# Kernel optimization log

Hardware: AMD Instinct MI355X
Metric: run time of the kernel (lower is better)

The kernel has to match this reference:

```python
import jax, jax.numpy as jnp
import numpy as np

B, SEQ, S, DIM_IN, DIM_K, DIM_V = 4, 2048, 128, 512, 64, 64
L = SEQ + 2 * S
NEG = -1e30  # stand-in for log(0) in the tril mask (finite for stable vjp)


def _layernorm(x, g, b, eps=1e-5):
    m = jnp.mean(x, axis=-1, keepdims=True)
    v = jnp.var(x, axis=-1, keepdims=True)
    return (x - m) / jnp.sqrt(v + eps) * g + b


def setup_inputs() -> dict:
    key = jax.random.key(0)
    ks = jax.random.split(key, 18)
    w = lambda k, shape, s=0.02: (jax.random.normal(k, shape, jnp.float32) * s)
    inp = {
        "x": jax.random.normal(ks[0], (B, L, DIM_IN), jnp.float32),
        "Wq": w(ks[1], (DIM_IN, DIM_K)),
        "Wk": w(ks[2], (DIM_IN, DIM_K)),
        "Wv": w(ks[3], (DIM_IN, DIM_V)),
        "Wq_s": w(ks[4], (DIM_IN, DIM_K)),
        "Wk_s": w(ks[5], (DIM_IN, DIM_K)),
        "Wv_s": w(ks[6], (DIM_IN, DIM_V)),
        "Wq_e": w(ks[7], (DIM_IN, DIM_K)),
        "Wk_e": w(ks[8], (DIM_IN, DIM_K)),
        "Wv_e": w(ks[9], (DIM_IN, DIM_V)),
        "ln_g": jnp.ones((DIM_IN,), jnp.float32),
        "ln_b": jnp.zeros((DIM_IN,), jnp.float32),
        "ln_s_g": jnp.ones((DIM_IN,), jnp.float32),
        "ln_s_b": jnp.zeros((DIM_IN,), jnp.float32),
        "ln_e_g": jnp.ones((DIM_IN,), jnp.float32),
        "ln_e_b": jnp.zeros((DIM_IN,), jnp.float32),
        "cope_emb": jax.random.normal(ks[10], (DIM_K, S), jnp.float32),
        "offset": 0,
    }
    return inp


def reference(x, Wq, Wk, Wv, Wq_s, Wk_s, Wv_s, Wq_e, Wk_e, Wv_e,
              ln_g, ln_b, ln_s_g, ln_s_b, ln_e_g, ln_e_b, cope_emb, offset):
    # extract_state: first/last state_len tokens
    xs, xm, xe = x[:, :S], x[:, S:L - S], x[:, -S:]
    xm = _layernorm(xm, ln_g, ln_b)
    xs = _layernorm(xs, ln_s_g, ln_s_b)
    xe = _layernorm(xe, ln_e_g, ln_e_b)

    q, k, v = xm @ Wq, xm @ Wk, xm @ Wv          # (B, SEQ, dk/dv)
    q_s, k_s, v_s = xs @ Wq_s, xs @ Wk_s, xs @ Wv_s
    q_e, k_e, v_e = xe @ Wq_e, xe @ Wk_e, xe @ Wv_e

    # CoPE bias over the non-state block
    logits = jnp.einsum('bqd,bkd->bqk', q, k)    # (B, SEQ, SEQ)
    gates = jax.nn.sigmoid(logits)
    pos = jnp.flip(jnp.cumsum(jnp.flip(gates, -1), axis=-1), -1)
    pos = jnp.minimum(pos, jnp.float32(S - 1))
    pos_ceil = jnp.ceil(pos).astype(jnp.int32)
    pos_floor = jnp.floor(pos).astype(jnp.int32)
    logits_int = jnp.einsum('bqd,dk->bqk', q, cope_emb)  # (B, SEQ, S)
    logits_c = jnp.take_along_axis(logits_int, pos_ceil, axis=-1)
    logits_f = jnp.take_along_axis(logits_int, pos_floor, axis=-1)
    wfrac = pos - pos_floor.astype(pos.dtype)
    bias = logits_c * wfrac + logits_f * (1.0 - wfrac)   # (B, SEQ, SEQ)

    q_full = jnp.concatenate([q_s, q, q_e], axis=1)      # (B, L, dk)
    k_full = jnp.concatenate([k_s, k, k_e], axis=1)
    v_full = jnp.concatenate([v_s, v, v_e], axis=1)

    # explicit tril log-mask bias with CoPE injected in the middle block
    tri = jnp.tril(jnp.ones((L, L), dtype=bool))
    attn_bias = jnp.where(tri, 0.0, NEG).astype(jnp.float32)
    attn_bias = jnp.broadcast_to(attn_bias, (B, L, L))
    attn_bias = attn_bias.at[:, S:L - S, S:L - S].add(bias)

    scale = 1.0 / jnp.sqrt(jnp.float32(DIM_K))
    scores = jnp.einsum('bqd,bkd->bqk', q_full, k_full) * scale + attn_bias
    att = jax.nn.softmax(scores, axis=-1)
    return jnp.einsum('bqk,bkd->bqd', att, v_full)       # (B, L, dv)
```

## Files before the change

kernel.cpp:

```cpp
#include <hip/hip_runtime.h>
#include <math.h>

#define B_    4
#define SEQ_  2048
#define S_    128
#define L_    2304
#define DIN   512
#define DK    64
#define NEGINF (-1e30f)
#define SCALE 0.125f
#define NCOLS 2176
#define NMID  8192
#define NEDGE 1024
#define LE    2304

typedef _Float16 f16;
typedef __attribute__((ext_vector_type(8))) _Float16 half8;
typedef __attribute__((ext_vector_type(4))) float f32x4;

union U4 { uint4 u; f16 h[8]; };

__global__ __launch_bounds__(256) void k_wsplit(
    const float* __restrict__ Wq,  const float* __restrict__ Wk,  const float* __restrict__ Wv,
    const float* __restrict__ Wqs, const float* __restrict__ Wks, const float* __restrict__ Wvs,
    const float* __restrict__ Wqe, const float* __restrict__ Wke, const float* __restrict__ Wve,
    f16* __restrict__ Wsp)
{
    __shared__ float xs[64 * 68];
    const int kt  = blockIdx.x;
    const int mat = blockIdx.y;
    const float* W;
    switch (mat) {
        case 0: W = Wq;  break; case 1: W = Wk;  break; case 2: W = Wv;  break;
        case 3: W = Wqs; break; case 4: W = Wks; break; case 5: W = Wvs; break;
        case 6: W = Wqe; break; case 7: W = Wke; break; default: W = Wve; break;
    }
    const int tid = threadIdx.x;
    const int k0  = kt * 64;
    #pragma unroll
    for (int i = 0; i < 4; ++i) {
        int g = tid + 256 * i;
        int k = g >> 4, c4 = g & 15;
        *(float4*)(xs + k * 68 + c4 * 4) = ((const float4*)W)[(size_t)(k0 + k) * 16 + c4];
    }
    __syncthreads();
    const int col = tid & 63, hf = tid >> 6;
    const int kk0 = hf * 16;
    U4 hi0, hi1, lo0, lo1;
    #pragma unroll
    for (int j = 0; j < 8; ++j) {
        float v0 = xs[(kk0 + j) * 68 + col];
        float v1 = xs[(kk0 + 8 + j) * 68 + col];
        hi0.h[j] = (f16)v0; lo0.h[j] = (f16)(v0 - (float)hi0.h[j]);
        hi1.h[j] = (f16)v1; lo1.h[j] = (f16)(v1 - (float)hi1.h[j]);
    }
    f16* dst = Wsp + (size_t)mat * 65536 + (size_t)col * 1024 + k0 + kk0;
    *(uint4*)(dst)       = hi0.u;
    *(uint4*)(dst + 8)   = hi1.u;
    *(uint4*)(dst + 512) = lo0.u;
    *(uint4*)(dst + 520) = lo1.u;
}

__global__ __launch_bounds__(256) void k_proj(
    const float* __restrict__ x, const f16* __restrict__ Wsp,
    const float* __restrict__ g0, const float* __restrict__ b0,
    const float* __restrict__ gs, const float* __restrict__ bs,
    const float* __restrict__ ge, const float* __restrict__ be,
    f16* __restrict__ qsp, f16* __restrict__ ksp, f16* __restrict__ vhT)
{
    __shared__ f16 As[32 * 136];
    __shared__ f16 Bs[3 * 64 * 136];
    __shared__ float mean_s[32], rstd_s[32];
    const int tid  = threadIdx.x;
    const int row0 = blockIdx.x * 32;
    const int rseq = row0 % L_;
    const int seg  = (rseq < S_) ? 0 : (rseq >= L_ - S_) ? 2 : 1;
    const int mat0 = (seg == 0) ? 3 : (seg == 2) ? 6 : 0;
    const float* gg = (seg == 0) ? gs : (seg == 2) ? ge : g0;
    const float* bb = (seg == 0) ? bs : (seg == 2) ? be : b0;

    {
        const int rr = tid >> 3, qq = tid & 7;
        const float4* xr = (const float4*)(x + (size_t)(row0 + rr) * DIN) + qq * 16;
        float s = 0.f, s2 = 0.f;
        #pragma unroll
        for (int i = 0; i < 16; ++i) {
            float4 v = xr[i];
            s  += v.x + v.y + v.z + v.w;
            s2 += v.x * v.x + v.y * v.y + v.z * v.z + v.w * v.w;
        }
        s  += __shfl_xor(s, 1);  s  += __shfl_xor(s, 2);  s  += __shfl_xor(s, 4);
        s2 += __shfl_xor(s2, 1); s2 += __shfl_xor(s2, 2); s2 += __shfl_xor(s2, 4);
        if (qq == 0) {
            float mean = s * (1.f / DIN);
            mean_s[rr] = mean;
            rstd_s[rr] = rsqrtf(s2 * (1.f / DIN) - mean * mean + 1e-5f);
        }
    }

    const int w = tid >> 6, lane = tid & 63;
    const int cl = lane & 15, quad = lane >> 4;
    const int r0 = 16 * (w >> 1), c0 = 32 * (w & 1);

    f32x4 acc[3][2];
    #pragma unroll
    for (int m = 0; m < 3; ++m)
        #pragma unroll
        for (int j = 0; j < 2; ++j) acc[m][j] = 0.f;

    for (int kc = 0; kc < DIN; kc += 64) {
        __syncthreads();
        {
            int r = tid >> 3, c8 = tid & 7;
            const float* xp = x + (size_t)(row0 + r) * DIN + kc + c8 * 8;
            float4 a0 = *(const float4*)xp;
            float4 a1 = *(const float4*)(xp + 4);
            float4 gA = *(const float4*)(gg + kc + c8 * 8);
            float4 gB = *(const float4*)(gg + kc + c8 * 8 + 4);
            float4 bA = *(const float4*)(bb + kc + c8 * 8);
            float4 bB = *(const float4*)(bb + kc + c8 * 8 + 4);
            float mean = mean_s[r], rstd = rstd_s[r];
            float n[8];
            n[0] = (a0.x - mean) * rstd * gA.x + bA.x;
            n[1] = (a0.y - mean) * rstd * gA.y + bA.y;
            n[2] = (a0.z - mean) * rstd * gA.z + bA.z;
            n[3] = (a0.w - mean) * rstd * gA.w + bA.w;
            n[4] = (a1.x - mean) * rstd * gB.x + bB.x;
            n[5] = (a1.y - mean) * rstd * gB.y + bB.y;
            n[6] = (a1.z - mean) * rstd * gB.z + bB.z;
            n[7] = (a1.w - mean) * rstd * gB.w + bB.w;
            U4 hi, lo;
            #pragma unroll
            for (int j = 0; j < 8; ++j) {
                hi.h[j] = (f16)n[j];
                lo.h[j] = (f16)(n[j] - (float)hi.h[j]);
            }
            *(uint4*)(As + r * 136 + c8 * 8)      = hi.u;
            *(uint4*)(As + r * 136 + 64 + c8 * 8) = lo.u;
        }
        #pragma unroll
        for (int i = 0; i < 6; ++i) {
            int g = tid + 256 * i;
            int mm = g >> 9, rem = g & 511;
            int col = rem >> 3, c8 = rem & 7;
            const f16* src = Wsp + (size_t)(mat0 + mm) * 65536 + (size_t)col * 1024 + kc + c8 * 8;
            f16* dst = Bs + mm * 8704 + col * 136 + c8 * 8;
            *(uint4*)(dst)      = *(const uint4*)(src);
            *(uint4*)(dst + 64) = *(const uint4*)(src + 512);
        }
        __syncthreads();
        #pragma unroll
        for (int h = 0; h < 2; ++h) {
            half8 ah, al;
            {
                const f16* base = As + (r0 + cl) * 136 + h * 32 + quad * 8;
                ah = *(const half8*)(base);
                al = *(const half8*)(base + 64);
            }
            #pragma unroll
            for (int m = 0; m < 3; ++m)
                #pragma unroll
                for (int cs = 0; cs < 2; ++cs) {
                    const f16* base = Bs + m * 8704 + (c0 + 16 * cs + cl) * 136 + h * 32 + quad * 8;
                    half8 bh = *(const half8*)(base);
                    half8 bl = *(const half8*)(base + 64);
                    acc[m][cs] = __builtin_amdgcn_mfma_f32_16x16x32_f16(ah, bh, acc[m][cs], 0, 0, 0);
                    acc[m][cs] = __builtin_amdgcn_mfma_f32_16x16x32_f16(ah, bl, acc[m][cs], 0, 0, 0);
                    acc[m][cs] = __builtin_amdgcn_mfma_f32_16x16x32_f16(al, bh, acc[m][cs], 0, 0, 0);
                }
        }
    }

    const int bI = row0 / L_;
    const int rb = row0 - bI * L_;
    #pragma unroll
    for (int m = 0; m < 3; ++m) {
        f16* sp = (m == 0) ? qsp : ksp;
        #pragma unroll
        for (int cs = 0; cs < 2; ++cs)
            #pragma unroll
            for (int r = 0; r < 4; ++r) {
                int lrow = r0 + quad * 4 + r;
                int col  = c0 + 16 * cs + cl;
                float v  = acc[m][cs][r];
                size_t grow = (size_t)(row0 + lrow);
                if (m < 2) {
                    f16 hv = (f16)v;
                    sp[grow * 128 + col]      = hv;
                    sp[grow * 128 + 64 + col] = (f16)(v - (float)hv);
                } else {
                    vhT[(size_t)(bI * 64 + col) * L_ + rb + lrow] = (f16)v;
                }
            }
    }
}

__global__ __launch_bounds__(256) void k_dots(
    const f16* __restrict__ qsp, const f16* __restrict__ ksp,
    float* __restrict__ D32, float* __restrict__ G, float* __restrict__ De32)
{
    const int bx = blockIdx.x, by = blockIdx.y;
    const bool edge = (bx >= 64);
    int b, q0 = 0;
    size_t qrow0;
    if (!edge) {
        if (by >= 17) return;
        b = bx >> 4;
        q0 = (bx * 128) & 2047;
        qrow0 = (size_t)b * L_ + S_ + q0;
    } else {
        int ex = bx - 64;
        b = ex >> 1;
        int half = ex & 1;
        if (half == 0 && by > 0) return;
        qrow0 = (size_t)b * L_ + (half ? 2176 : 0);
    }
    const int col0 = by * 128;
    const size_t krow0 = (size_t)b * L_ + col0;

    __shared__ f16 Qs[128 * 136];
    __shared__ f16 Ks[128 * 136];
    const int tid = threadIdx.x;

    #pragma unroll
    for (int i = 0; i < 8; ++i) {
        int g = tid + 256 * i;
        int r = g >> 4, c = g & 15;
        *(uint4*)(Qs + r * 136 + c * 8) = *(const uint4*)(qsp + (qrow0 + r) * 128 + c * 8);
        *(uint4*)(Ks + r * 136 + c * 8) = *(const uint4*)(ksp + (krow0 + r) * 128 + c * 8);
    }
    __syncthreads();

    const int w = tid >> 6, lane = tid & 63;
    const int cl = lane & 15, quad = lane >> 4;

    f32x4 acc[2][8];
    #pragma unroll
    for (int i = 0; i < 2; ++i)
        #pragma unroll
        for (int j = 0; j < 8; ++j) acc[i][j] = 0.f;

    #pragma unroll
    for (int h = 0; h < 2; ++h) {
        half8 ah[2], al[2];
        #pragma unroll
        for (int rs = 0; rs < 2; ++rs) {
            const f16* base = Qs + (32 * w + 16 * rs + cl) * 136 + h * 32 + quad * 8;
            ah[rs] = *(const half8*)(base);
            al[rs] = *(const half8*)(base + 64);
        }
        #pragma unroll
        for (int cq = 0; cq < 2; ++cq) {
            half8 bh[4], bl[4];
            #pragma unroll
            for (int cc = 0; cc < 4; ++cc) {
                const f16* base = Ks + (16 * (cq * 4 + cc) + cl) * 136 + h * 32 + quad * 8;
                bh[cc] = *(const half8*)(base);
                bl[cc] = *(const half8*)(base + 64);
            }
            #pragma unroll
            for (int rs = 0; rs < 2; ++rs)
                #pragma unroll
                for (int cc = 0; cc < 4; ++cc) {
                    int c = cq * 4 + cc;
                    acc[rs][c] = __builtin_amdgcn_mfma_f32_16x16x32_f16(ah[rs], bh[cc], acc[rs][c], 0, 0, 0);
                    acc[rs][c] = __builtin_amdgcn_mfma_f32_16x16x32_f16(ah[rs], bl[cc], acc[rs][c], 0, 0, 0);
                    acc[rs][c] = __builtin_amdgcn_mfma_f32_16x16x32_f16(al[rs], bh[cc], acc[rs][c], 0, 0, 0);
                }
        }
    }

    if (!edge) {
        const int gr0 = bx * 128;
        const bool writeD = (by == 0) || ((by - 1) <= (q0 >> 7));
        if (writeD) {
            #pragma unroll
            for (int rs = 0; rs < 2; ++rs)
                #pragma unroll
                for (int c = 0; c < 8; ++c)
                    #pragma unroll
                    for (int r = 0; r < 4; ++r) {
                        int mrow = gr0 + 32 * w + 16 * rs + quad * 4 + r;
                        int n    = col0 + 16 * c + cl;
                        D32[(size_t)mrow * NCOLS + n] = acc[rs][c][r];
                    }
        }
        if (by >= 1) {
            const int chm = 2 * (by - 1);
            #pragma unroll
            for (int rs = 0; rs < 2; ++rs)
                #pragma unroll
                for (int r = 0; r < 4; ++r) {
                    float sA = 0.f, sB = 0.f;
                    #pragma unroll
                    for (int cc = 0; cc < 4; ++cc) {
                        sA += 1.f / (1.f + __expf(-acc[rs][cc][r]));
                        sB += 1.f / (1.f + __expf(-acc[rs][4 + cc][r]));
                    }
                    #pragma unroll
                    for (int off = 1; off < 16; off <<= 1) {
                        sA += __shfl_xor(sA, off);
                        sB += __shfl_xor(sB, off);
                    }
                    if (cl == 0) {
                        int row = gr0 + 32 * w + 16 * rs + quad * 4 + r;
                        G[(size_t)row * 32 + chm]     = sA;
                        G[(size_t)row * 32 + chm + 1] = sB;
                    }
                }
        }
    } else {
        const int er0 = (bx - 64) * 128;
        #pragma unroll
        for (int rs = 0; rs < 2; ++rs)
            #pragma unroll
            for (int c = 0; c < 8; ++c)
                #pragma unroll
                for (int r = 0; r < 4; ++r) {
                    int erow = er0 + 32 * w + 16 * rs + quad * 4 + r;
                    int n    = col0 + 16 * c + cl;
                    De32[(size_t)erow * LE + n] = acc[rs][c][r];
                }
    }
}

__global__ __launch_bounds__(256) void k_scan(
    const f16* __restrict__ qsp, const float* __restrict__ cope,
    const float* __restrict__ G,
    const float* __restrict__ D32, f16* __restrict__ Dp,
    const float* __restrict__ De32, f16* __restrict__ Dep)
{
    __shared__ f16   qvh[128];
    __shared__ float li[128];
    __shared__ float Gs[32];
    __shared__ float Gsf[32];
    __shared__ float wmax[4], wsum[4];
    const int tid = threadIdx.x;
    const int gr  = blockIdx.x;
    const int lane = tid & 63, wid = tid >> 6;

    if (gr < NMID) {
        const int b = gr >> 11;
        const int q = gr & 2047;
        const size_t grow = (size_t)b * L_ + S_ + q;
        const int qlim = (q & ~63) + 64;

        if (tid < 16) ((uint4*)qvh)[tid] = ((const uint4*)(qsp + grow * 128))[tid];
        if (tid >= 16 && tid < 24)
            ((float4*)Gs)[tid - 16] = ((const float4*)G)[(size_t)gr * 8 + tid - 16];
        __syncthreads();
        if (tid < 128) {
            float a = 0.f;
            #pragma unroll
            for (int d = 0; d < DK; ++d)
                a += ((float)qvh[d] + (float)qvh[64 + d]) * cope[d * S_ + tid];
            li[tid] = a;
        }
        if (tid >= 128 && tid < 160) {
            int c = tid - 128;
            float s = 0.f;
            for (int cc = c + 1; cc < 32; ++cc) s += Gs[cc];
            Gsf[c] = s;
        }

        const float* Sr = D32 + (size_t)gr * NCOLS;
        f16* Dr = Dp + (size_t)gr * NCOLS;
        const int j0 = tid * 8;
        const int cg = tid >> 3, sl = tid & 7;
        float dot[8], gte[8];
        float csum = 0.f;
        if (j0 < qlim) {
            float4 t0 = *(const float4*)(Sr + 128 + j0);
            float4 t1 = *(const float4*)(Sr + 128 + j0 + 4);
            dot[0] = t0.x; dot[1] = t0.y; dot[2] = t0.z; dot[3] = t0.w;
            dot[4] = t1.x; dot[5] = t1.y; dot[6] = t1.z; dot[7] = t1.w;
            #pragma unroll
            for (int jj = 0; jj < 8; ++jj) {
                gte[jj] = 1.f / (1.f + __expf(-dot[jj]));
                csum += gte[jj];
            }
        } else {
            #pragma unroll
            for (int jj = 0; jj < 8; ++jj) { dot[jj] = 0.f; gte[jj] = 0.f; }
        }
        float sv = (tid < 128) ? Sr[tid] * SCALE : NEGINF;

        float inc = csum;
        #pragma unroll
        for (int off = 1; off < 8; off <<= 1) {
            float u = __shfl_down(inc, off, 8);
            if (sl + off < 8) inc += u;
        }
        __syncthreads();
        float run = (inc - csum) + Gsf[cg];

        float p8[8];
        #pragma unroll
        for (int jj = 7; jj >= 0; --jj) {
            run += gte[jj];
            float pos = fminf(run, (float)(S_ - 1));
            float pfl = floorf(pos);
            int ic  = (int)ceilf(pos);
            int ifl = (int)pfl;
            float w = pos - pfl;
            float bias = li[ic] * w + li[ifl] * (1.f - w);
            p8[jj] = (j0 + jj <= q) ? dot[jj] * SCALE + bias : NEGINF;
        }

        float mx = sv;
        #pragma unroll
        for (int jj = 0; jj < 8; ++jj) mx = fmaxf(mx, p8[jj]);
        #pragma unroll
        for (int off = 1; off < 64; off <<= 1) mx = fmaxf(mx, __shfl_xor(mx, off));
        if (lane == 0) wmax[wid] = mx;
        __syncthreads();
        mx = fmaxf(fmaxf(wmax[0], wmax[1]), fmaxf(wmax[2], wmax[3]));

        float lsum = 0.f;
        float e8[8];
        #pragma unroll
        for (int jj = 0; jj < 8; ++jj) {
            e8[jj] = __expf(p8[jj] - mx);
            lsum += e8[jj];
        }
        float es = 0.f;
        if (tid < 128) { es = __expf(sv - mx); lsum += es; }
        #pragma unroll
        for (int off = 1; off < 64; off <<= 1) lsum += __shfl_xor(lsum, off);
        if (lane == 0) wsum[wid] = lsum;
        __syncthreads();
        float inv = 1.f / (wsum[0] + wsum[1] + wsum[2] + wsum[3]);

        if (j0 < qlim) {
            U4 o;
            #pragma unroll
            for (int jj = 0; jj < 8; ++jj) o.h[jj] = (f16)(e8[jj] * inv);
            *(uint4*)(Dr + 128 + j0) = o.u;
        }
        if (tid < 128) Dr[tid] = (f16)(es * inv);
    } else {
        const int er = gr - NMID;
        const int r  = er & 255;
        const int Q  = (r < 128) ? r : (2048 + r);
        const float* Er32 = De32 + (size_t)er * LE;
        f16* Er = Dep + (size_t)er * LE;

        float v[9];
        #pragma unroll
        for (int i = 0; i < 9; ++i) {
            int j = tid + 256 * i;
            float d = Er32[j];
            v[i] = (j <= Q) ? d * SCALE : NEGINF;
        }
        float mx = v[0];
        #pragma unroll
        for (int i = 1; i < 9; ++i) mx = fmaxf(mx, v[i]);
        #pragma unroll
        for (int off = 1; off < 64; off <<= 1) mx = fmaxf(mx, __shfl_xor(mx, off));
        if (lane == 0) wmax[wid] = mx;
        __syncthreads();
        mx = fmaxf(fmaxf(wmax[0], wmax[1]), fmaxf(wmax[2], wmax[3]));

        float lsum = 0.f;
        #pragma unroll
        for (int i = 0; i < 9; ++i) {
            v[i] = __expf(v[i] - mx);
            lsum += v[i];
        }
        #pragma unroll
        for (int off = 1; off < 64; off <<= 1) lsum += __shfl_xor(lsum, off);
        if (lane == 0) wsum[wid] = lsum;
        __syncthreads();
        float inv = 1.f / (wsum[0] + wsum[1] + wsum[2] + wsum[3]);

        #pragma unroll
        for (int i = 0; i < 9; ++i)
            Er[tid + 256 * i] = (f16)(v[i] * inv);
    }
}

__global__ __launch_bounds__(256) void k_pv(
    const f16* __restrict__ Pmid, const f16* __restrict__ Pedge,
    const f16* __restrict__ vhT,
    float* __restrict__ Opart, float* __restrict__ Oe)
{
    __shared__ f16 Ps[64 * 72];
    __shared__ f16 Vt[64 * 72];
    const int tid = threadIdx.x;
    const int bx  = blockIdx.x;
    const int ks  = blockIdx.y;
    const bool edge = (bx >= 128);

    const f16* Pb;
    size_t pitch;
    int row0, b, cap, cmax;
    float* outp;
    if (!edge) {
        row0 = bx * 64;
        b = row0 >> 11;
        int q0 = row0 & 2047;
        Pb = Pmid; pitch = NCOLS; cap = 34;
        cmax = (191 + q0) >> 6;
        outp = Opart + (size_t)ks * NMID * DK;
    } else {
        row0 = (bx - 128) * 64;
        b = row0 >> 8;
        int r0 = row0 & 255;
        Pb = Pedge; pitch = LE; cap = 36;
        int Qmax = (r0 < 128) ? (r0 + 63) : (2048 + r0 + 63);
        cmax = Qmax >> 6;
        outp = Oe + (size_t)ks * NEDGE * DK;
    }
    const int c_beg = ks * 9;
    int c_end = c_beg + 9;
    if (c_end > cap) c_end = cap;
    if (c_end > cmax + 1) c_end = cmax + 1;

    const int w = tid >> 6, lane = tid & 63;
    const int cl = lane & 15, quad = lane >> 4;
    f32x4 acc[4];
    #pragma unroll
    for (int c = 0; c < 4; ++c) acc[c] = 0.f;

    for (int ch = c_beg; ch < c_end; ++ch) {
        __syncthreads();
        #pragma unroll
        for (int i = 0; i < 2; ++i) {
            int g = tid + 256 * i;
            int r = g >> 3, c = g & 7;
            *(uint4*)(Ps + r * 72 + c * 8) =
                *(const uint4*)(Pb + (size_t)(row0 + r) * pitch + ch * 64 + c * 8);
            *(uint4*)(Vt + r * 72 + c * 8) =
                *(const uint4*)(vhT + (size_t)(b * 64 + r) * L_ + ch * 64 + c * 8);
        }
        __syncthreads();
        #pragma unroll
        for (int h = 0; h < 2; ++h) {
            half8 a = *(const half8*)(Ps + (16 * w + cl) * 72 + h * 32 + quad * 8);
            #pragma unroll
            for (int c = 0; c < 4; ++c) {
                half8 bv = *(const half8*)(Vt + (16 * c + cl) * 72 + h * 32 + quad * 8);
                acc[c] = __builtin_amdgcn_mfma_f32_16x16x32_f16(a, bv, acc[c], 0, 0, 0);
            }
        }
    }
    #pragma unroll
    for (int c = 0; c < 4; ++c)
        #pragma unroll
        for (int r = 0; r < 4; ++r) {
            int mrow = row0 + 16 * w + quad * 4 + r;
            int n    = 16 * c + cl;
            outp[(size_t)mrow * DK + n] = acc[c][r];
        }
}

__global__ __launch_bounds__(256) void k_merge(
    const float* __restrict__ Opart, const float* __restrict__ Oe,
    float* __restrict__ out)
{
    const int e = blockIdx.x * 256 + threadIdx.x;
    if (e < NMID * DK) {
        const int gr = e >> 6, c = e & 63;
        const int b  = gr >> 11, q = gr & 2047;
        const int NP = NMID * DK;
        float s = Opart[e] + Opart[e + NP] + Opart[e + 2 * NP] + Opart[e + 3 * NP];
        out[((size_t)b * L_ + S_ + q) * DK + c] = s;
    } else {
        const int e2 = e - NMID * DK;
        const int er = e2 >> 6, c = e2 & 63;
        const int b  = er >> 8, r = er & 255;
        const int gQ = (r < 128) ? r : (2048 + r);
        const int NP = NEDGE * DK;
        float s = Oe[e2] + Oe[e2 + NP] + Oe[e2 + 2 * NP] + Oe[e2 + 3 * NP];
        out[((size_t)b * L_ + gQ) * DK + c] = s;
    }
}

extern "C" void kernel_launch(void* const* d_in, const int* in_sizes, int n_in,
                              void* d_out, int out_size, void* d_ws, size_t ws_size,
                              hipStream_t stream)
{
    const float* x    = (const float*)d_in[0];
    const float* Wq   = (const float*)d_in[1];
    const float* Wk   = (const float*)d_in[2];
    const float* Wv   = (const float*)d_in[3];
    const float* Wqs  = (const float*)d_in[4];
    const float* Wks  = (const float*)d_in[5];
    const float* Wvs  = (const float*)d_in[6];
    const float* Wqe  = (const float*)d_in[7];
    const float* Wke  = (const float*)d_in[8];
    const float* Wve  = (const float*)d_in[9];
    const float* g0   = (const float*)d_in[10];
    const float* b0   = (const float*)d_in[11];
    const float* gs   = (const float*)d_in[12];
    const float* bs   = (const float*)d_in[13];
    const float* ge   = (const float*)d_in[14];
    const float* be   = (const float*)d_in[15];
    const float* cope = (const float*)d_in[16];

    const size_t NR = (size_t)B_ * L_;
    f16*   qsp   = (f16*)d_ws;
    f16*   ksp   = qsp + NR * 128;
    f16*   vhT   = ksp + NR * 128;
    f16*   Wsp   = vhT + NR * 64;
    float* G     = (float*)(Wsp + (size_t)9 * 65536);
    float* Opart = G + (size_t)NMID * 32;
    float* Oe    = Opart + (size_t)4 * NMID * DK;
    float* Dm32  = Oe + (size_t)4 * NEDGE * DK;
    float* De32  = Dm32 + (size_t)NMID * NCOLS;
    f16*   Dp    = (f16*)(De32 + (size_t)NEDGE * LE);
    f16*   Dep   = Dp + (size_t)NMID * NCOLS;
    float* out   = (float*)d_out;

    k_wsplit<<<dim3(8, 9), 256, 0, stream>>>(Wq, Wk, Wv, Wqs, Wks, Wvs,
                                             Wqe, Wke, Wve, Wsp);
    k_proj<<<288, 256, 0, stream>>>(x, Wsp, g0, b0, gs, bs, ge, be,
                                    qsp, ksp, vhT);
    k_dots<<<dim3(72, 18), 256, 0, stream>>>(qsp, ksp, Dm32, G, De32);
    k_scan<<<NMID + NEDGE, 256, 0, stream>>>(qsp, cope, G, Dm32, Dp, De32, Dep);
    k_pv  <<<dim3(144, 4), 256, 0, stream>>>(Dp, Dep, vhT, Opart, Oe);
    k_merge<<<(NMID + NEDGE) * DK / 256, 256, 0, stream>>>(Opart, Oe, out);
}
```

Measured before the change: 194.6 us.

## Fuse middle-block QK, CoPE gating scan, softmax and PV into flash-style kernel

Replaces the middle-block pipeline of score materialisation, gate sums, scan, softmax and PV with one streaming kernel. It walks key tiles from right to left, keeps a running reverse-cumsum of sigmoid gates, and does an online softmax with PV accumulation in registers. CoPE interpolation logits are computed per strip via MFMA against a pre-split cope matrix. This removes the large fp32/fp16 score buffers and their global traffic. The cost is only 256 blocks, many barriers per tile, and non-causal tiles still loaded for the gate scan.

Result: slower. 227.9 us (+17.1%).

```diff
diff --git a/kernel.cpp b/kernel.cpp
--- a/kernel.cpp
+++ b/kernel.cpp
@@ -24,18 +24,46 @@
     const float* __restrict__ Wq,  const float* __restrict__ Wk,  const float* __restrict__ Wv,
     const float* __restrict__ Wqs, const float* __restrict__ Wks, const float* __restrict__ Wvs,
     const float* __restrict__ Wqe, const float* __restrict__ Wke, const float* __restrict__ Wve,
-    f16* __restrict__ Wsp)
+    const float* __restrict__ cope,
+    f16* __restrict__ Wsp, f16* __restrict__ copesp)
 {
     __shared__ float xs[64 * 68];
     const int kt  = blockIdx.x;
     const int mat = blockIdx.y;
+    const int tid = threadIdx.x;
+
+    if (mat == 9) {
+        if (kt != 0) return;
+        for (int half = 0; half < 2; ++half) {
+            #pragma unroll
+            for (int i = 0; i < 4; ++i) {
+                int g = tid + 256 * i;
+                int d = g >> 4, p4 = g & 15;
+                *(float4*)(xs + d * 68 + p4 * 4) =
+                    *(const float4*)(cope + (size_t)d * 128 + half * 64 + p4 * 4);
+            }
+            __syncthreads();
+            if (tid < 128) {
+                int pp = tid & 63, hf = tid >> 6;
+                int d0 = hf * 32;
+                for (int j = 0; j < 32; ++j) {
+                    float v = xs[(d0 + j) * 68 + pp];
+                    f16 hi = (f16)v;
+                    copesp[(size_t)(half * 64 + pp) * 128 + d0 + j]      = hi;
+                    copesp[(size_t)(half * 64 + pp) * 128 + 64 + d0 + j] = (f16)(v - (float)hi);
+                }
+            }
+            __syncthreads();
+        }
+        return;
+    }
+
     const float* W;
     switch (mat) {
         case 0: W = Wq;  break; case 1: W = Wk;  break; case 2: W = Wv;  break;
         case 3: W = Wqs; break; case 4: W = Wks; break; case 5: W = Wvs; break;
         case 6: W = Wqe; break; case 7: W = Wke; break; default: W = Wve; break;
     }
-    const int tid = threadIdx.x;
     const int k0  = kt * 64;
     #pragma unroll
     for (int i = 0; i < 4; ++i) {
@@ -195,26 +223,250 @@
     }
 }
 
-__global__ __launch_bounds__(256) void k_dots(
+__global__ __launch_bounds__(512) void k_fmid(
     const f16* __restrict__ qsp, const f16* __restrict__ ksp,
-    float* __restrict__ D32, float* __restrict__ G, float* __restrict__ De32)
-{
-    const int bx = blockIdx.x, by = blockIdx.y;
-    const bool edge = (bx >= 64);
-    int b, q0 = 0;
-    size_t qrow0;
-    if (!edge) {
-        if (by >= 17) return;
-        b = bx >> 4;
-        q0 = (bx * 128) & 2047;
-        qrow0 = (size_t)b * L_ + S_ + q0;
-    } else {
-        int ex = bx - 64;
-        b = ex >> 1;
-        int half = ex & 1;
-        if (half == 0 && by > 0) return;
-        qrow0 = (size_t)b * L_ + (half ? 2176 : 0);
-    }
+    const f16* __restrict__ vhT, const f16* __restrict__ copesp,
+    float* __restrict__ out)
+{
+    __shared__ f16 Qs[32 * 136];
+    __shared__ f16 Ks[128 * 136];
+    __shared__ f16 Vt[64 * 136];
+    __shared__ float li[32 * 132];
+    __shared__ float Tq[4][32], Tm[4][32], Ll[4][32];
+    f16* const Ps = Ks + 64 * 136;
+
+    const int tid = threadIdx.x;
+    const int blk = blockIdx.x;
+    const int b = blk >> 6, strip = blk & 63;
+    const int q0 = strip * 32;
+    const size_t rowbase = (size_t)b * L_ + S_ + q0;
+    const int w = tid >> 6, lane = tid & 63;
+    const int cl = lane & 15, quad = lane >> 4;
+    const int g = w >> 2, ch = w & 3;
+    const int tmax = ((q0 + 31) >> 7) + 1;
+
+    {
+        int r = tid >> 4, c = tid & 15;
+        *(uint4*)(Qs + r * 136 + c * 8) = *(const uint4*)(qsp + (rowbase + r) * 128 + c * 8);
+    }
+    __syncthreads();
+
+    {
+        f32x4 accli[2];
+        accli[0] = 0.f; accli[1] = 0.f;
+        #pragma unroll
+        for (int h = 0; h < 2; ++h) {
+            const f16* abase = Qs + (16 * g + cl) * 136 + h * 32 + quad * 8;
+            half8 ah = *(const half8*)(abase);
+            half8 al = *(const half8*)(abase + 64);
+            #pragma unroll
+            for (int cf = 0; cf < 2; ++cf) {
+                const f16* bbase = copesp + (size_t)(32 * ch + 16 * cf + cl) * 128 + h * 32 + quad * 8;
+                half8 bh = *(const half8*)(bbase);
+                half8 bl = *(const half8*)(bbase + 64);
+                accli[cf] = __builtin_amdgcn_mfma_f32_16x16x32_f16(ah, bh, accli[cf], 0, 0, 0);
+                accli[cf] = __builtin_amdgcn_mfma_f32_16x16x32_f16(ah, bl, accli[cf], 0, 0, 0);
+                accli[cf] = __builtin_amdgcn_mfma_f32_16x16x32_f16(al, bh, accli[cf], 0, 0, 0);
+            }
+        }
+        #pragma unroll
+        for (int cf = 0; cf < 2; ++cf)
+            #pragma unroll
+            for (int r = 0; r < 4; ++r)
+                li[(16 * g + quad * 4 + r) * 132 + 32 * ch + 16 * cf + cl] = accli[cf][r];
+    }
+
+    float R[4]  = {0.f, 0.f, 0.f, 0.f};
+    float m_run[4] = {NEGINF, NEGINF, NEGINF, NEGINF};
+    float l_run[4] = {0.f, 0.f, 0.f, 0.f};
+    f32x4 accO = 0.f;
+
+    for (int t = 16; t >= 0; --t) {
+        const bool mid    = (t >= 1);
+        const bool causal = (t <= tmax);
+        const int kbase   = mid ? (S_ + 128 * (t - 1)) : 0;
+
+        __syncthreads();
+        #pragma unroll
+        for (int i = 0; i < 4; ++i) {
+            int gi = tid + 512 * i;
+            int r = gi >> 4, c = gi & 15;
+            *(uint4*)(Ks + r * 136 + c * 8) =
+                *(const uint4*)(ksp + ((size_t)b * L_ + kbase + r) * 128 + c * 8);
+        }
+        if (causal) {
+            #pragma unroll
+            for (int i = 0; i < 2; ++i) {
+                int gi = tid + 512 * i;
+                int vc = gi >> 4, c = gi & 15;
+                *(uint4*)(Vt + vc * 136 + c * 8) =
+                    *(const uint4*)(vhT + (size_t)(b * 64 + vc) * L_ + kbase + c * 8);
+            }
+        }
+        __syncthreads();
+
+        f32x4 acc[2];
+        acc[0] = 0.f; acc[1] = 0.f;
+        #pragma unroll
+        for (int h = 0; h < 2; ++h) {
+            const f16* abase = Qs + (16 * g + cl) * 136 + h * 32 + quad * 8;
+            half8 ah = *(const half8*)(abase);
+            half8 al = *(const half8*)(abase + 64);
+            #pragma unroll
+            for (int cf = 0; cf < 2; ++cf) {
+                const f16* bbase = Ks + (32 * ch + 16 * cf + cl) * 136 + h * 32 + quad * 8;
+                half8 bh = *(const half8*)(bbase);
+                half8 bl = *(const half8*)(bbase + 64);
+                acc[cf] = __builtin_amdgcn_mfma_f32_16x16x32_f16(ah, bh, acc[cf], 0, 0, 0);
+                acc[cf] = __builtin_amdgcn_mfma_f32_16x16x32_f16(ah, bl, acc[cf], 0, 0, 0);
+                acc[cf] = __builtin_amdgcn_mfma_f32_16x16x32_f16(al, bh, acc[cf], 0, 0, 0);
+            }
+        }
+
+        float sfx[2][4], F1r[4];
+        float hq[4], ttot[4];
+        if (mid) {
+            #pragma unroll
+            for (int cf = 0; cf < 2; ++cf)
+                #pragma unroll
+                for (int r = 0; r < 4; ++r)
+                    sfx[cf][r] = 1.f / (1.f + __expf(-acc[cf][r]));
+            #pragma unroll
+            for (int off = 1; off < 16; off <<= 1) {
+                #pragma unroll
+                for (int cf = 0; cf < 2; ++cf)
+                    #pragma unroll
+                    for (int r = 0; r < 4; ++r) {
+                        float u = __shfl_down(sfx[cf][r], off, 16);
+                        if (cl + off < 16) sfx[cf][r] += u;
+                    }
+            }
+            float F0r[4];
+            #pragma unroll
+            for (int r = 0; r < 4; ++r) {
+                F0r[r] = __shfl(sfx[0][r], 0, 16);
+                F1r[r] = __shfl(sfx[1][r], 0, 16);
+            }
+            if (cl == 0) {
+                #pragma unroll
+                for (int r = 0; r < 4; ++r)
+                    Tq[ch][16 * g + quad * 4 + r] = F0r[r] + F1r[r];
+            }
+            __syncthreads();
+            #pragma unroll
+            for (int r = 0; r < 4; ++r) {
+                int row = 16 * g + quad * 4 + r;
+                float t0 = Tq[0][row], t1 = Tq[1][row], t2 = Tq[2][row], t3 = Tq[3][row];
+                ttot[r] = t0 + t1 + t2 + t3;
+                hq[r] = (ch == 0) ? (t1 + t2 + t3) : (ch == 1) ? (t2 + t3) : (ch == 2) ? t3 : 0.f;
+            }
+        }
+
+        if (causal) {
+            float p0[2][4];
+            float ml[4] = {NEGINF, NEGINF, NEGINF, NEGINF};
+            #pragma unroll
+            for (int cf = 0; cf < 2; ++cf)
+                #pragma unroll
+                for (int r = 0; r < 4; ++r) {
+                    int row = 16 * g + quad * 4 + r;
+                    int q = q0 + row;
+                    float sc;
+                    if (mid) {
+                        int mcol = 128 * (t - 1) + 32 * ch + 16 * cf + cl;
+                        float run = sfx[cf][r] + ((cf == 0) ? F1r[r] : 0.f) + hq[r] + R[r];
+                        float pos = fminf(run, 127.f);
+                        float pfl = floorf(pos);
+                        int ic = (int)ceilf(pos), ifl = (int)pfl;
+                        float wf = pos - pfl;
+                        float bias = li[row * 132 + ic] * wf + li[row * 132 + ifl] * (1.f - wf);
+                        sc = (mcol <= q) ? acc[cf][r] * SCALE + bias : NEGINF;
+                    } else {
+                        sc = acc[cf][r] * SCALE;
+                    }
+                    p0[cf][r] = sc;
+                    ml[r] = fmaxf(ml[r], sc);
+                }
+            #pragma unroll
+            for (int off = 1; off < 16; off <<= 1)
+                #pragma unroll
+                for (int r = 0; r < 4; ++r)
+                    ml[r] = fmaxf(ml[r], __shfl_xor(ml[r], off, 16));
+            if (cl == 0) {
+                #pragma unroll
+                for (int r = 0; r < 4; ++r)
+                    Tm[ch][16 * g + quad * 4 + r] = ml[r];
+            }
+            __syncthreads();
+            float rs_[4];
+            #pragma unroll
+            for (int r = 0; r < 4; ++r) {
+                int row = 16 * g + quad * 4 + r;
+                float mn = fmaxf(fmaxf(Tm[0][row], Tm[1][row]), fmaxf(Tm[2][row], Tm[3][row]));
+                mn = fmaxf(fmaxf(mn, m_run[r]), -1e28f);
+                rs_[r] = __expf(m_run[r] - mn);
+                m_run[r] = mn;
+            }
+            float ll[4] = {0.f, 0.f, 0.f, 0.f};
+            #pragma unroll
+            for (int cf = 0; cf < 2; ++cf)
+                #pragma unroll
+                for (int r = 0; r < 4; ++r) {
+                    int row = 16 * g + quad * 4 + r;
+                    float e = __expf(p0[cf][r] - m_run[r]);
+                    ll[r] += e;
+                    Ps[row * 136 + 32 * ch + 16 * cf + cl] = (f16)e;
+                }
+            #pragma unroll
+            for (int off = 1; off < 16; off <<= 1)
+                #pragma unroll
+                for (int r = 0; r < 4; ++r)
+                    ll[r] += __shfl_xor(ll[r], off, 16);
+            if (cl == 0) {
+                #pragma unroll
+                for (int r = 0; r < 4; ++r)
+                    Ll[ch][16 * g + quad * 4 + r] = ll[r];
+            }
+            #pragma unroll
+            for (int r = 0; r < 4; ++r) accO[r] *= rs_[r];
+            __syncthreads();
+            #pragma unroll
+            for (int r = 0; r < 4; ++r) {
+                int row = 16 * g + quad * 4 + r;
+                l_run[r] = l_run[r] * rs_[r] + Ll[0][row] + Ll[1][row] + Ll[2][row] + Ll[3][row];
+            }
+            #pragma unroll
+            for (int kf = 0; kf < 4; ++kf) {
+                half8 a  = *(const half8*)(Ps + (16 * g + cl) * 136 + kf * 32 + quad * 8);
+                half8 bv = *(const half8*)(Vt + (16 * ch + cl) * 136 + kf * 32 + quad * 8);
+                accO = __builtin_amdgcn_mfma_f32_16x16x32_f16(a, bv, accO, 0, 0, 0);
+            }
+        }
+
+        if (mid) {
+            #pragma unroll
+            for (int r = 0; r < 4; ++r) R[r] += ttot[r];
+        }
+    }
+
+    #pragma unroll
+    for (int r = 0; r < 4; ++r) {
+        int row = 16 * g + quad * 4 + r;
+        int col = 16 * ch + cl;
+        out[(rowbase + row) * DK + col] = accO[r] / l_run[r];
+    }
+}
+
+__global__ __launch_bounds__(256) void k_dotse(
+    const f16* __restrict__ qsp, const f16* __restrict__ ksp,
+    float* __restrict__ De32)
+{
+    const int bx = blockIdx.x + 64, by = blockIdx.y;
+    int ex = bx - 64;
+    int b = ex >> 1;
+    int half = ex & 1;
+    if (half == 0 && by > 0) return;
+    size_t qrow0 = (size_t)b * L_ + (half ? 2176 : 0);
     const int col0 = by * 128;
     const size_t krow0 = (size_t)b * L_ + col0;
 
@@ -270,250 +522,85 @@
         }
     }
 
-    if (!edge) {
-        const int gr0 = bx * 128;
-        const bool writeD = (by == 0) || ((by - 1) <= (q0 >> 7));
-        if (writeD) {
-            #pragma unroll
-            for (int rs = 0; rs < 2; ++rs)
-                #pragma unroll
-                for (int c = 0; c < 8; ++c)
-                    #pragma unroll
-                    for (int r = 0; r < 4; ++r) {
-                        int mrow = gr0 + 32 * w + 16 * rs + quad * 4 + r;
-                        int n    = col0 + 16 * c + cl;
-                        D32[(size_t)mrow * NCOLS + n] = acc[rs][c][r];
-                    }
-        }
-        if (by >= 1) {
-            const int chm = 2 * (by - 1);
-            #pragma unroll
-            for (int rs = 0; rs < 2; ++rs)
-                #pragma unroll
-                for (int r = 0; r < 4; ++r) {
-                    float sA = 0.f, sB = 0.f;
-                    #pragma unroll
-                    for (int cc = 0; cc < 4; ++cc) {
-                        sA += 1.f / (1.f + __expf(-acc[rs][cc][r]));
-                        sB += 1.f / (1.f + __expf(-acc[rs][4 + cc][r]));
-                    }
-                    #pragma unroll
-                    for (int off = 1; off < 16; off <<= 1) {
-                        sA += __shfl_xor(sA, off);
-                        sB += __shfl_xor(sB, off);
-                    }
-                    if (cl == 0) {
-                        int row = gr0 + 32 * w + 16 * rs + quad * 4 + r;
-                        G[(size_t)row * 32 + chm]     = sA;
-                        G[(size_t)row * 32 + chm + 1] = sB;
-                    }
-                }
-        }
-    } else {
-        const int er0 = (bx - 64) * 128;
-        #pragma unroll
-        for (int rs = 0; rs < 2; ++rs)
-            #pragma unroll
-            for (int c = 0; c < 8; ++c)
-                #pragma unroll
-                for (int r = 0; r < 4; ++r) {
-                    int erow = er0 + 32 * w + 16 * rs + quad * 4 + r;
-                    int n    = col0 + 16 * c + cl;
-                    De32[(size_t)erow * LE + n] = acc[rs][c][r];
-                }
-    }
-}
-
-__global__ __launch_bounds__(256) void k_scan(
-    const f16* __restrict__ qsp, const float* __restrict__ cope,
-    const float* __restrict__ G,
-    const float* __restrict__ D32, f16* __restrict__ Dp,
+    const int er0 = (bx - 64) * 128;
+    #pragma unroll
+    for (int rs = 0; rs < 2; ++rs)
+        #pragma unroll
+        for (int c = 0; c < 8; ++c)
+            #pragma unroll
+            for (int r = 0; r < 4; ++r) {
+                int erow = er0 + 32 * w + 16 * rs + quad * 4 + r;
+                int n    = col0 + 16 * c + cl;
+                De32[(size_t)erow * LE + n] = acc[rs][c][r];
+            }
+}
+
+__global__ __launch_bounds__(256) void k_scane(
     const float* __restrict__ De32, f16* __restrict__ Dep)
 {
-    __shared__ f16   qvh[128];
-    __shared__ float li[128];
-    __shared__ float Gs[32];
-    __shared__ float Gsf[32];
     __shared__ float wmax[4], wsum[4];
     const int tid = threadIdx.x;
-    const int gr  = blockIdx.x;
+    const int er  = blockIdx.x;
     const int lane = tid & 63, wid = tid >> 6;
-
-    if (gr < NMID) {
-        const int b = gr >> 11;
-        const int q = gr & 2047;
-        const size_t grow = (size_t)b * L_ + S_ + q;
-        const int qlim = (q & ~63) + 64;
-
-        if (tid < 16) ((uint4*)qvh)[tid] = ((const uint4*)(qsp + grow * 128))[tid];
-        if (tid >= 16 && tid < 24)
-            ((float4*)Gs)[tid - 16] = ((const float4*)G)[(size_t)gr * 8 + tid - 16];
-        __syncthreads();
-        if (tid < 128) {
-            float a = 0.f;
-            #pragma unroll
-            for (int d = 0; d < DK; ++d)
-                a += ((float)qvh[d] + (float)qvh[64 + d]) * cope[d * S_ + tid];
-            li[tid] = a;
-        }
-        if (tid >= 128 && tid < 160) {
-            int c = tid - 128;
-            float s = 0.f;
-            for (int cc = c + 1; cc < 32; ++cc) s += Gs[cc];
-            Gsf[c] = s;
-        }
-
-        const float* Sr = D32 + (size_t)gr * NCOLS;
-        f16* Dr = Dp + (size_t)gr * NCOLS;
-        const int j0 = tid * 8;
-        const int cg = tid >> 3, sl = tid & 7;
-        float dot[8], gte[8];
-        float csum = 0.f;
-        if (j0 < qlim) {
-            float4 t0 = *(const float4*)(Sr + 128 + j0);
-            float4 t1 = *(const float4*)(Sr + 128 + j0 + 4);
-            dot[0] = t0.x; dot[1] = t0.y; dot[2] = t0.z; dot[3] = t0.w;
-            dot[4] = t1.x; dot[5] = t1.y; dot[6] = t1.z; dot[7] = t1.w;
-            #pragma unroll
-            for (int jj = 0; jj < 8; ++jj) {
-                gte[jj] = 1.f / (1.f + __expf(-dot[jj]));
-                csum += gte[jj];
-            }
-        } else {
-            #pragma unroll
-            for (int jj = 0; jj < 8; ++jj) { dot[jj] = 0.f; gte[jj] = 0.f; }
-        }
-        float sv = (tid < 128) ? Sr[tid] * SCALE : NEGINF;
-
-        float inc = csum;
-        #pragma unroll
-        for (int off = 1; off < 8; off <<= 1) {
-            float u = __shfl_down(inc, off, 8);
-            if (sl + off < 8) inc += u;
-        }
-        __syncthreads();
-        float run = (inc - csum) + Gsf[cg];
-
-        float p8[8];
-        #pragma unroll
-        for (int jj = 7; jj >= 0; --jj) {
-            run += gte[jj];
-            float pos = fminf(run, (float)(S_ - 1));
-            float pfl = floorf(pos);
-            int ic  = (int)ceilf(pos);
-            int ifl = (int)pfl;
-            float w = pos - pfl;
-            float bias = li[ic] * w + li[ifl] * (1.f - w);
-            p8[jj] = (j0 + jj <= q) ? dot[jj] * SCALE + bias : NEGINF;
-        }
-
-        float mx = sv;
-        #pragma unroll
-        for (int jj = 0; jj < 8; ++jj) mx = fmaxf(mx, p8[jj]);
-        #pragma unroll
-        for (int off = 1; off < 64; off <<= 1) mx = fmaxf(mx, __shfl_xor(mx, off));
-        if (lane == 0) wmax[wid] = mx;
-        __syncthreads();
-        mx = fmaxf(fmaxf(wmax[0], wmax[1]), fmaxf(wmax[2], wmax[3]));
-
-        float lsum = 0.f;
-        float e8[8];
-        #pragma unroll
-        for (int jj = 0; jj < 8; ++jj) {
-            e8[jj] = __expf(p8[jj] - mx);
-            lsum += e8[jj];
-        }
-        float es = 0.f;
-        if (tid < 128) { es = __expf(sv - mx); lsum += es; }
-        #pragma unroll
-        for (int off = 1; off < 64; off <<= 1) lsum += __shfl_xor(lsum, off);
-        if (lane == 0) wsum[wid] = lsum;
-        __syncthreads();
-        float inv = 1.f / (wsum[0] + wsum[1] + wsum[2] + wsum[3]);
-
-        if (j0 < qlim) {
-            U4 o;
-            #pragma unroll
-            for (int jj = 0; jj < 8; ++jj) o.h[jj] = (f16)(e8[jj] * inv);
-            *(uint4*)(Dr + 128 + j0) = o.u;
-        }
-        if (tid < 128) Dr[tid] = (f16)(es * inv);
-    } else {
-        const int er = gr - NMID;
-        const int r  = er & 255;
-        const int Q  = (r < 128) ? r : (2048 + r);
-        const float* Er32 = De32 + (size_t)er * LE;
-        f16* Er = Dep + (size_t)er * LE;
-
-        float v[9];
-        #pragma unroll
-        for (int i = 0; i < 9; ++i) {
-            int j = tid + 256 * i;
-            float d = Er32[j];
-            v[i] = (j <= Q) ? d * SCALE : NEGINF;
-        }
-        float mx = v[0];
-        #pragma unroll
-        for (int i = 1; i < 9; ++i) mx = fmaxf(mx, v[i]);
-        #pragma unroll
-        for (int off = 1; off < 64; off <<= 1) mx = fmaxf(mx, __shfl_xor(mx, off));
-        if (lane == 0) wmax[wid] = mx;
-        __syncthreads();
-        mx = fmaxf(fmaxf(wmax[0], wmax[1]), fmaxf(wmax[2], wmax[3]));
-
-        float lsum = 0.f;
-        #pragma unroll
-        for (int i = 0; i < 9; ++i) {
-            v[i] = __expf(v[i] - mx);
-            lsum += v[i];
-        }
-        #pragma unroll
-        for (int off = 1; off < 64; off <<= 1) lsum += __shfl_xor(lsum, off);
-        if (lane == 0) wsum[wid] = lsum;
-        __syncthreads();
-        float inv = 1.f / (wsum[0] + wsum[1] + wsum[2] + wsum[3]);
-
-        #pragma unroll
-        for (int i = 0; i < 9; ++i)
-            Er[tid + 256 * i] = (f16)(v[i] * inv);
-    }
-}
-
-__global__ __launch_bounds__(256) void k_pv(
-    const f16* __restrict__ Pmid, const f16* __restrict__ Pedge,
-    const f16* __restrict__ vhT,
-    float* __restrict__ Opart, float* __restrict__ Oe)
+    const int r  = er & 255;
+    const int Q  = (r < 128) ? r : (2048 + r);
+    const float* Er32 = De32 + (size_t)er * LE;
+    f16* Er = Dep + (size_t)er * LE;
+
+    float v[9];
+    #pragma unroll
+    for (int i = 0; i < 9; ++i) {
+        int j = tid + 256 * i;
+        float d = Er32[j];
+        v[i] = (j <= Q) ? d * SCALE : NEGINF;
+    }
+    float mx = v[0];
+    #pragma unroll
+    for (int i = 1; i < 9; ++i) mx = fmaxf(mx, v[i]);
+    #pragma unroll
+    for (int off = 1; off < 64; off <<= 1) mx = fmaxf(mx, __shfl_xor(mx, off));
+    if (lane == 0) wmax[wid] = mx;
+    __syncthreads();
+    mx = fmaxf(fmaxf(wmax[0], wmax[1]), fmaxf(wmax[2], wmax[3]));
+
+    float lsum = 0.f;
+    #pragma unroll
+    for (int i = 0; i < 9; ++i) {
+        v[i] = __expf(v[i] - mx);
+        lsum += v[i];
+    }
+    #pragma unroll
+    for (int off = 1; off < 64; off <<= 1) lsum += __shfl_xor(lsum, off);
+    if (lane == 0) wsum[wid] = lsum;
+    __syncthreads();
+    float inv = 1.f / (wsum[0] + wsum[1] + wsum[2] + wsum[3]);
+
+    #pragma unroll
+    for (int i = 0; i < 9; ++i)
+        Er[tid + 256 * i] = (f16)(v[i] * inv);
+}
+
+__global__ __launch_bounds__(256) void k_pve(
+    const f16* __restrict__ Pedge, const f16* __restrict__ vhT,
+    float* __restrict__ Oe)
 {
     __shared__ f16 Ps[64 * 72];
     __shared__ f16 Vt[64 * 72];
     const int tid = threadIdx.x;
-    const int bx  = blockIdx.x;
     const int ks  = blockIdx.y;
-    const bool edge = (bx >= 128);
-
-    const f16* Pb;
-    size_t pitch;
-    int row0, b, cap, cmax;
-    float* outp;
-    if (!edge) {
-        row0 = bx * 64;
-        b = row0 >> 11;
-        int q0 = row0 & 2047;
-        Pb = Pmid; pitch = NCOLS; cap = 34;
-        cmax = (191 + q0) >> 6;
-        outp = Opart + (size_t)ks * NMID * DK;
-    } else {
-        row0 = (bx - 128) * 64;
-        b = row0 >> 8;
-        int r0 = row0 & 255;
-        Pb = Pedge; pitch = LE; cap = 36;
-        int Qmax = (r0 < 128) ? (r0 + 63) : (2048 + r0 + 63);
-        cmax = Qmax >> 6;
-        outp = Oe + (size_t)ks * NEDGE * DK;
-    }
+
+    int row0 = blockIdx.x * 64;
+    int b = row0 >> 8;
+    int r0 = row0 & 255;
+    const f16* Pb = Pedge;
+    const size_t pitch = LE;
+    int Qmax = (r0 < 128) ? (r0 + 63) : (2048 + r0 + 63);
+    int cmax = Qmax >> 6;
+    float* outp = Oe + (size_t)ks * NEDGE * DK;
+
     const int c_beg = ks * 9;
     int c_end = c_beg + 9;
-    if (c_end > cap) c_end = cap;
+    if (c_end > 36) c_end = 36;
     if (c_end > cmax + 1) c_end = cmax + 1;
 
     const int w = tid >> 6, lane = tid & 63;
@@ -554,26 +641,16 @@
         }
 }
 
-__global__ __launch_bounds__(256) void k_merge(
-    const float* __restrict__ Opart, const float* __restrict__ Oe,
-    float* __restrict__ out)
-{
-    const int e = blockIdx.x * 256 + threadIdx.x;
-    if (e < NMID * DK) {
-        const int gr = e >> 6, c = e & 63;
-        const int b  = gr >> 11, q = gr & 2047;
-        const int NP = NMID * DK;
-        float s = Opart[e] + Opart[e + NP] + Opart[e + 2 * NP] + Opart[e + 3 * NP];
-        out[((size_t)b * L_ + S_ + q) * DK + c] = s;
-    } else {
-        const int e2 = e - NMID * DK;
-        const int er = e2 >> 6, c = e2 & 63;
-        const int b  = er >> 8, r = er & 255;
-        const int gQ = (r < 128) ? r : (2048 + r);
-        const int NP = NEDGE * DK;
-        float s = Oe[e2] + Oe[e2 + NP] + Oe[e2 + 2 * NP] + Oe[e2 + 3 * NP];
-        out[((size_t)b * L_ + gQ) * DK + c] = s;
-    }
+__global__ __launch_bounds__(256) void k_mergee(
+    const float* __restrict__ Oe, float* __restrict__ out)
+{
+    const int e2 = blockIdx.x * 256 + threadIdx.x;
+    const int er = e2 >> 6, c = e2 & 63;
+    const int b  = er >> 8, r = er & 255;
+    const int gQ = (r < 128) ? r : (2048 + r);
+    const int NP = NEDGE * DK;
+    float s = Oe[e2] + Oe[e2 + NP] + Oe[e2 + 2 * NP] + Oe[e2 + 3 * NP];
+    out[((size_t)b * L_ + gQ) * DK + c] = s;
 }
 
 extern "C" void kernel_launch(void* const* d_in, const int* in_sizes, int n_in,
@@ -599,25 +676,23 @@
     const float* cope = (const float*)d_in[16];
 
     const size_t NR = (size_t)B_ * L_;
-    f16*   qsp   = (f16*)d_ws;
-    f16*   ksp   = qsp + NR * 128;
-    f16*   vhT   = ksp + NR * 128;
-    f16*   Wsp   = vhT + NR * 64;
-    float* G     = (float*)(Wsp + (size_t)9 * 65536);
-    float* Opart = G + (size_t)NMID * 32;
-    float* Oe    = Opart + (size_t)4 * NMID * DK;
-    float* Dm32  = Oe + (size_t)4 * NEDGE * DK;
-    float* De32  = Dm32 + (size_t)NMID * NCOLS;
-    f16*   Dp    = (f16*)(De32 + (size_t)NEDGE * LE);
-    f16*   Dep   = Dp + (size_t)NMID * NCOLS;
-    float* out   = (float*)d_out;
-
-    k_wsplit<<<dim3(8, 9), 256, 0, stream>>>(Wq, Wk, Wv, Wqs, Wks, Wvs,
-                                             Wqe, Wke, Wve, Wsp);
+    f16*   qsp    = (f16*)d_ws;
+    f16*   ksp    = qsp + NR * 128;
+    f16*   vhT    = ksp + NR * 128;
+    f16*   Wsp    = vhT + NR * 64;
+    f16*   copesp = Wsp + (size_t)9 * 65536;
+    float* De32   = (float*)(copesp + 16384);
+    float* Oe     = De32 + (size_t)NEDGE * LE;
+    f16*   Dep    = (f16*)(Oe + (size_t)4 * NEDGE * DK);
+    float* out    = (float*)d_out;
+
+    k_wsplit<<<dim3(8, 10), 256, 0, stream>>>(Wq, Wk, Wv, Wqs, Wks, Wvs,
+                                              Wqe, Wke, Wve, cope, Wsp, copesp);
     k_proj<<<288, 256, 0, stream>>>(x, Wsp, g0, b0, gs, bs, ge, be,
                                     qsp, ksp, vhT);
-    k_dots<<<dim3(72, 18), 256, 0, stream>>>(qsp, ksp, Dm32, G, De32);
-    k_scan<<<NMID + NEDGE, 256, 0, stream>>>(qsp, cope, G, Dm32, Dp, De32, Dep);
-    k_pv  <<<dim3(144, 4), 256, 0, stream>>>(Dp, Dep, vhT, Opart, Oe);
-    k_merge<<<(NMID + NEDGE) * DK / 256, 256, 0, stream>>>(Opart, Oe, out);
-}
+    k_dotse<<<dim3(8, 18), 256, 0, stream>>>(qsp, ksp, De32);
+    k_fmid<<<256, 512, 0, stream>>>(qsp, ksp, vhT, copesp, out);
+    k_scane<<<NEDGE, 256, 0, stream>>>(De32, Dep);
+    k_pve<<<dim3(16, 4), 256, 0, stream>>>(Dep, vhT, Oe);
+    k_mergee<<<256, 256, 0, stream>>>(Oe, out);
+}
```
